# Kernel tuning notes

Hardware: AMD Instinct MI355X
Metric: run time of the kernel (lower is better)

Reference implementation:

```python
import jax, jax.numpy as jnp
import numpy as np


def _maxpool2(t):
    # 2x2 max pool, stride 2. t: [B, C, H, W]
    B, C, H, W = t.shape
    return t.reshape(B, C, H // 2, 2, W // 2, 2).max(axis=(3, 5))


def setup_inputs() -> dict:
    key = jax.random.key(0)
    ks = jax.random.split(key, 5)
    B, C, H, W = 4, 64, 128, 128
    x = jax.random.normal(ks[0], (B, C, H, W), dtype=jnp.float32)
    w_theta = jax.random.normal(ks[1], (C // 8, C), dtype=jnp.float32) * (1.0 / np.sqrt(C))
    w_phi = jax.random.normal(ks[2], (C // 8, C), dtype=jnp.float32) * (1.0 / np.sqrt(C))
    w_g = jax.random.normal(ks[3], (C // 2, C), dtype=jnp.float32) * (1.0 / np.sqrt(C))
    w_o = jax.random.normal(ks[4], (C, C // 2), dtype=jnp.float32) * (1.0 / np.sqrt(C // 2))
    gamma = jnp.ones((1,), dtype=jnp.float32)
    return {"x": x, "w_theta": w_theta, "w_phi": w_phi, "w_g": w_g, "w_o": w_o, "gamma": gamma}


def reference(x, w_theta, w_phi, w_g, w_o, gamma):
    B, C, H, W = x.shape
    N = H * W
    # 1x1 convs (bias-free) are channel matmuls
    theta = jnp.einsum('oc,bchw->bohw', w_theta, x)            # [B, C/8, H, W]
    phi = _maxpool2(jnp.einsum('oc,bchw->bohw', w_phi, x))     # [B, C/8, H/2, W/2]
    g = _maxpool2(jnp.einsum('oc,bchw->bohw', w_g, x))         # [B, C/2, H/2, W/2]
    theta = theta.reshape(B, C // 8, N)                        # [B, C/8, N]
    phi = phi.reshape(B, C // 8, N // 4)                       # [B, C/8, N/4]
    g = g.reshape(B, C // 2, N // 4)                           # [B, C/2, N/4]
    # attention: no 1/sqrt(d) scaling in SAGAN
    scores = jnp.einsum('bcn,bcm->bnm', theta, phi)            # [B, N, N/4]
    beta = jax.nn.softmax(scores, axis=-1)
    attn = jnp.einsum('bcm,bnm->bcn', g, beta)                 # [B, C/2, N]
    o = jnp.einsum('oc,bcn->bon', w_o, attn).reshape(B, C, H, W)
    return gamma[0] * o + x
```

## Files before the change

### kernel.cpp

```cpp
#include <hip/hip_runtime.h>
#include <hip/hip_bf16.h>


typedef __attribute__((ext_vector_type(16))) float f32x16;
typedef __attribute__((ext_vector_type(4))) float f32x4;
typedef __attribute__((ext_vector_type(2))) float f32x2;
typedef __attribute__((ext_vector_type(8))) short s16x8;

__device__ __forceinline__ unsigned short f32_bf16(float f) {
    unsigned int u = __float_as_uint(f);
    return (unsigned short)((u + 0x7fffu + ((u >> 16) & 1u)) >> 16);
}
__device__ __forceinline__ unsigned int pk_bf16(float a, float b) {
    return (unsigned int)f32_bf16(a) | ((unsigned int)f32_bf16(b) << 16);
}
__device__ __forceinline__ unsigned int pk_rh(float a, float b) {
    unsigned int au = __float_as_uint(a) + 0x8000u;
    unsigned int bu = __float_as_uint(b) + 0x8000u;
    return __builtin_amdgcn_perm(bu, au, 0x07060302u);
}
__device__ __forceinline__ unsigned int pk_tr(float a, float b) {
    return __builtin_amdgcn_perm(__float_as_uint(b), __float_as_uint(a), 0x07060302u);
}
__device__ __forceinline__ void async16(const void* g, void* l) {
    __builtin_amdgcn_global_load_lds(
        (const __attribute__((address_space(1))) unsigned int*)g,
        (__attribute__((address_space(3))) unsigned int*)l, 16, 0, 0);
}

__global__ __launch_bounds__(256) void proj_kernel(
    const float* __restrict__ x,
    const float* __restrict__ w_theta, const float* __restrict__ w_phi,
    const float* __restrict__ w_g,
    __hip_bfloat16* __restrict__ thG,
    __hip_bfloat16* __restrict__ phG,
    __hip_bfloat16* __restrict__ gG)
{
    __shared__ __align__(16) unsigned short x_s[128 * 72];
    int tid = threadIdx.x;
    int bx = blockIdx.x;
    int b = bx >> 7, mh = (bx >> 1) & 63, ph = bx & 1;

    {
        int cp = tid >> 3, s = tid & 7;
        const float* xb = x + ((size_t)b << 20) + (size_t)(2 * mh) * 128 + 64 * ph;
        const float* p0r = xb + ((size_t)(2 * cp) << 14);
        const float* p1r = p0r + (1 << 14);
#pragma unroll
        for (int py = 0; py < 2; py++)
#pragma unroll
            for (int t = 0; t < 2; t++) {
                int pxl = 4 * s + 32 * t;
                float4 a = *(const float4*)(p0r + py * 128 + pxl);
                float4 c = *(const float4*)(p1r + py * 128 + pxl);
                int pix = py * 64 + pxl;
                *(unsigned int*)&x_s[(pix + 0) * 72 + 2 * cp] = pk_rh(a.x, c.x);
                *(unsigned int*)&x_s[(pix + 1) * 72 + 2 * cp] = pk_rh(a.y, c.y);
                *(unsigned int*)&x_s[(pix + 2) * 72 + 2 * cp] = pk_rh(a.z, c.z);
                *(unsigned int*)&x_s[(pix + 3) * 72 + 2 * cp] = pk_rh(a.w, c.w);
            }
    }

    int lane = tid & 63, w = tid >> 6;
    int q = lane >> 4, nl = lane & 15;

    s16x8 A[3][2];
#pragma unroll
    for (int CT = 0; CT < 3; CT++) {
        const float* wsrc;
        float scale = 1.0f;
        if (CT == 0) {
            if (nl < 8) { wsrc = w_theta + nl * 64; scale = 1.44269504f; }
            else        { wsrc = w_phi + (nl - 8) * 64; }
        } else if (CT == 1) wsrc = w_g + nl * 64;
        else                wsrc = w_g + (16 + nl) * 64;
#pragma unroll
        for (int ks = 0; ks < 2; ks++) {
            const float4* p4 = (const float4*)(wsrc + 32 * ks + 8 * q);
            float4 a0 = p4[0], a1 = p4[1];
            s16x8 f;
            f[0] = (short)f32_bf16(a0.x * scale); f[1] = (short)f32_bf16(a0.y * scale);
            f[2] = (short)f32_bf16(a0.z * scale); f[3] = (short)f32_bf16(a0.w * scale);
            f[4] = (short)f32_bf16(a1.x * scale); f[5] = (short)f32_bf16(a1.y * scale);
            f[6] = (short)f32_bf16(a1.z * scale); f[7] = (short)f32_bf16(a1.w * scale);
            A[CT][ks] = f;
        }
    }
    __syncthreads();

    f32x4 acc[3][2];
#pragma unroll
    for (int ti = 0; ti < 2; ti++) {
        int tile = w + 4 * ti;
        const unsigned short* rb = x_s + (16 * tile + nl) * 72;
        s16x8 B0 = *(const s16x8*)(rb + 8 * q);
        s16x8 B1 = *(const s16x8*)(rb + 32 + 8 * q);
#pragma unroll
        for (int CT = 0; CT < 3; CT++) {
            f32x4 d = (f32x4){0.f, 0.f, 0.f, 0.f};
            d = __builtin_amdgcn_mfma_f32_16x16x32_bf16(A[CT][0], B0, d, 0, 0, 0);
            d = __builtin_amdgcn_mfma_f32_16x16x32_bf16(A[CT][1], B1, d, 0, 0, 0);
            acc[CT][ti] = d;
        }
    }

    if (q < 2) {
        unsigned short* thb = (unsigned short*)thG + ((size_t)b << 14) * 8;
#pragma unroll
        for (int ti = 0; ti < 2; ti++) {
            int n = (2 * mh + ti) * 128 + 64 * ph + 16 * w + nl;
            uint2 tv;
            tv.x = pk_bf16(acc[0][ti][0], acc[0][ti][1]);
            tv.y = pk_bf16(acc[0][ti][2], acc[0][ti][3]);
            *(uint2*)(thb + (size_t)n * 8 + 4 * q) = tv;
        }
    }

    float pool[3][4];
#pragma unroll
    for (int CT = 0; CT < 3; CT++)
#pragma unroll
        for (int r = 0; r < 4; r++) {
            float a = fmaxf(acc[CT][0][r], acc[CT][1][r]);
            pool[CT][r] = fmaxf(a, __shfl_xor(a, 1));
        }

    int mm = 8 * w + (nl >> 1);
    int mbase = mh * 64 + ph * 32;
    if ((nl & 1) == 0) {
        if (q >= 2) {
            uint2 pv;
            pv.x = pk_bf16(pool[0][0], pool[0][1]);
            pv.y = pk_bf16(pool[0][2], pool[0][3]);
            *(uint2*)((unsigned short*)phG + ((size_t)(b * 4096 + mbase + mm)) * 8 + (q - 2) * 4) = pv;
        }
        int p = 16 * ((mm >> 4) & 1) + 8 * ((mm >> 2) & 1) + 4 * ((mm >> 3) & 1) + (mm & 3);
        int mstore = mbase + p;
#pragma unroll
        for (int CT = 1; CT < 3; CT++)
#pragma unroll
            for (int r = 0; r < 4; r++) {
                int cg = 16 * (CT - 1) + 4 * q + r;
                ((unsigned short*)gG)[((size_t)(b * 32 + cg) << 12) + mstore] =
                    f32_bf16(pool[CT][r]);
            }
    }
}

__global__ __launch_bounds__(256) void attn_kernel(
    const __hip_bfloat16* __restrict__ thG, const __hip_bfloat16* __restrict__ phG,
    const __hip_bfloat16* __restrict__ gG,
    const float* __restrict__ w_o, const float* __restrict__ gamma,
    const float* __restrict__ x, float* __restrict__ out)
{
    __shared__ __align__(16) unsigned char smem[2 * 16384 + 2 * 4096];
    unsigned char* O_s = smem;

    int tid = threadIdx.x, lane = tid & 63, w = tid >> 6;
    int q = lane >> 4, nl = lane & 15;
    int c31 = lane & 31, h = lane >> 5;
    int bx = blockIdx.x;
    int b  = bx >> 7;
    int n0 = (bx & 127) << 7;
    int nw = n0 + w * 32;

    const unsigned short* thb = (const unsigned short*)thG + ((size_t)b << 14) * 8;
    const unsigned short* phb = (const unsigned short*)phG + ((size_t)b << 12) * 8;
    const unsigned short* ggb = (const unsigned short*)gG + ((size_t)b << 17);

    s16x8 BT = (s16x8){0, 0, 0, 0, 0, 0, 0, 0};
    if (h == 0) BT = *(const s16x8*)(thb + (size_t)(nw + c31) * 8);
    else        BT[0] = (short)0xC167;
    s16x8 Fc = (s16x8){0, 0, 0, 0, 0, 0, 0, 0};
    if (h == 1) Fc[0] = (short)0x3F80;

    f32x16 acc = {};
    f32x2  l2 = (f32x2){0.f, 0.f};

    int r0 = 8 * w + (lane >> 5);
    const unsigned short* gsrc0 = ggb + ((size_t)(r0 + 0) << 12) + 8 * ((lane & 31) ^ (r0 + 0));
    const unsigned short* gsrc1 = ggb + ((size_t)(r0 + 2) << 12) + 8 * ((lane & 31) ^ (r0 + 2));
    const unsigned short* gsrc2 = ggb + ((size_t)(r0 + 4) << 12) + 8 * ((lane & 31) ^ (r0 + 4));
    const unsigned short* gsrc3 = ggb + ((size_t)(r0 + 6) << 12) + 8 * ((lane & 31) ^ (r0 + 6));
    const unsigned short* psrc  = phb + (size_t)(w * 64 + lane) * 8;
    unsigned char* ldsg0 = smem + w * 4096;
    unsigned char* ldsg1 = ldsg0 + 1024;
    unsigned char* ldsg2 = ldsg0 + 2048;
    unsigned char* ldsg3 = ldsg0 + 3072;
    unsigned char* ldsp  = smem + 32768 + w * 1024;

    async16(gsrc0, ldsg0);
    async16(gsrc1, ldsg1);
    async16(gsrc2, ldsg2);
    async16(gsrc3, ldsg3);
    async16(psrc, ldsp);
    __syncthreads();

    for (int st = 0; st < 16; st++) {
        const unsigned char* gcur = smem + (st & 1) * 16384;
        const unsigned char* pcur = smem + 32768 + (st & 1) * 4096;
        if (st < 15) {
            int mo = (st + 1) << 8;
            int nb = (st + 1) & 1;
            async16(gsrc0 + mo, ldsg0 + nb * 16384);
            async16(gsrc1 + mo, ldsg1 + nb * 16384);
            async16(gsrc2 + mo, ldsg2 + nb * 16384);
            async16(gsrc3 + mo, ldsg3 + nb * 16384);
            async16(psrc + (size_t)mo * 8, ldsp + nb * 4096);
        }
#pragma unroll
        for (int t8 = 0; t8 < 8; t8++) {
            int mloc = t8 << 5;
            s16x8 F = Fc;
            if (h == 0) F = *(const s16x8*)(pcur + (mloc + c31) * 16);
            int s0 = (t8 << 2) + h;
            s16x8 G1 = *(const s16x8*)(gcur + c31 * 512 + (((s0 + 0) ^ c31) << 4));
            s16x8 G2 = *(const s16x8*)(gcur + c31 * 512 + (((s0 + 2) ^ c31) << 4));

            f32x16 z = {};
            f32x16 S = __builtin_amdgcn_mfma_f32_32x32x16_bf16(F, BT, z, 0, 0, 0);

            float p0  = __builtin_amdgcn_exp2f(S[0]);
            float p1  = __builtin_amdgcn_exp2f(S[1]);
            float p2  = __builtin_amdgcn_exp2f(S[2]);
            float p3  = __builtin_amdgcn_exp2f(S[3]);
            float p4  = __builtin_amdgcn_exp2f(S[4]);
            float p5  = __builtin_amdgcn_exp2f(S[5]);
            float p6  = __builtin_amdgcn_exp2f(S[6]);
            float p7  = __builtin_amdgcn_exp2f(S[7]);
            float p8  = __builtin_amdgcn_exp2f(S[8]);
            float p9  = __builtin_amdgcn_exp2f(S[9]);
            float p10 = __builtin_amdgcn_exp2f(S[10]);
            float p11 = __builtin_amdgcn_exp2f(S[11]);
            float p12 = __builtin_amdgcn_exp2f(S[12]);
            float p13 = __builtin_amdgcn_exp2f(S[13]);
            float p14 = __builtin_amdgcn_exp2f(S[14]);
            float p15 = __builtin_amdgcn_exp2f(S[15]);

            f32x2 u0 = (f32x2){p0, p1} + (f32x2){p2, p3};
            f32x2 u1 = (f32x2){p4, p5} + (f32x2){p6, p7};
            f32x2 u2 = (f32x2){p8, p9} + (f32x2){p10, p11};
            f32x2 u3 = (f32x2){p12, p13} + (f32x2){p14, p15};
            l2 += (u0 + u1) + (u2 + u3);

            uint4 ub1 = make_uint4(pk_tr(p0, p1), pk_tr(p2, p3),
                                   pk_tr(p4, p5), pk_tr(p6, p7));
            uint4 ub2 = make_uint4(pk_tr(p8, p9), pk_tr(p10, p11),
                                   pk_tr(p12, p13), pk_tr(p14, p15));
            s16x8 B1 = *(s16x8*)&ub1;
            s16x8 B2 = *(s16x8*)&ub2;

            acc = __builtin_amdgcn_mfma_f32_32x32x16_bf16(G1, B1, acc, 0, 0, 0);
            acc = __builtin_amdgcn_mfma_f32_32x32x16_bf16(G2, B2, acc, 0, 0, 0);
        }
        __syncthreads();
    }

    float l = l2[0] + l2[1];
    l += __shfl_xor(l, 32);
    float linv = 1.0f / l;
    acc *= linv;

    s16x8 WO[4];
#pragma unroll
    for (int g4 = 0; g4 < 4; g4++) {
        const float4* wr = (const float4*)(w_o + (size_t)(g4 * 16 + nl) * 32 + q * 8);
        float4 a0 = wr[0], a1 = wr[1];
        WO[g4][0] = (short)f32_bf16(a0.x); WO[g4][1] = (short)f32_bf16(a0.y);
        WO[g4][2] = (short)f32_bf16(a0.z); WO[g4][3] = (short)f32_bf16(a0.w);
        WO[g4][4] = (short)f32_bf16(a1.x); WO[g4][5] = (short)f32_bf16(a1.y);
        WO[g4][6] = (short)f32_bf16(a1.z); WO[g4][7] = (short)f32_bf16(a1.w);
    }
    float gam = gamma[0];

    int nloc = w * 32 + c31;
    {
#pragma unroll
        for (int g2 = 0; g2 < 4; g2++) {
            uint2 ov;
            ov.x = pk_bf16(acc[4 * g2 + 0], acc[4 * g2 + 1]);
            ov.y = pk_bf16(acc[4 * g2 + 2], acc[4 * g2 + 3]);
            *(uint2*)(O_s + nloc * 80 + 16 * g2 + 8 * h) = ov;
        }
    }
    int nloc0 = w * 32 + nl;
    int nloc1 = nloc0 + 16;
    s16x8 OB0 = *(const s16x8*)(O_s + nloc0 * 80 + q * 16);
    s16x8 OB1 = *(const s16x8*)(O_s + nloc1 * 80 + q * 16);
#pragma unroll
    for (int g4 = 0; g4 < 4; g4++) {
        f32x4 e0 = (f32x4){0.f, 0.f, 0.f, 0.f};
        f32x4 e1 = (f32x4){0.f, 0.f, 0.f, 0.f};
        e0 = __builtin_amdgcn_mfma_f32_16x16x32_bf16(WO[g4], OB0, e0, 0, 0, 0);
        e1 = __builtin_amdgcn_mfma_f32_16x16x32_bf16(WO[g4], OB1, e1, 0, 0, 0);
#pragma unroll
        for (int r = 0; r < 4; r++) {
            int cc = g4 * 16 + q * 4 + r;
            size_t gi0 = (((size_t)(b * 64 + cc)) << 14) + nw + nl;
            out[gi0] = gam * e0[r] + x[gi0];
            size_t gi1 = gi0 + 16;
            out[gi1] = gam * e1[r] + x[gi1];
        }
    }
}

extern "C" void kernel_launch(void* const* d_in, const int* in_sizes, int n_in,
                              void* d_out, int out_size, void* d_ws, size_t ws_size,
                              hipStream_t stream) {
    const float* x       = (const float*)d_in[0];
    const float* w_theta = (const float*)d_in[1];
    const float* w_phi   = (const float*)d_in[2];
    const float* w_g     = (const float*)d_in[3];
    const float* w_o     = (const float*)d_in[4];
    const float* gamma   = (const float*)d_in[5];
    float* out = (float*)d_out;

    __hip_bfloat16* thG = (__hip_bfloat16*)d_ws;
    __hip_bfloat16* phG = thG + 524288;
    __hip_bfloat16* gG  = phG + 131072;

    proj_kernel<<<512, 256, 0, stream>>>(x, w_theta, w_phi, w_g, thG, phG, gG);
    attn_kernel<<<512, 256, 0, stream>>>(thG, phG, gG, w_o, gamma, x, out);
}
```

Baseline: 127.5 us.

## Split attention key range across two wave groups per block and merge via LDS

The attention kernel now launches 512 threads per block, with two halves of four waves each processing half of the key/value range (split-K) for the same 128 query rows. Each half keeps its own double-buffered G/phi tiles in LDS, and at the end the second half writes its accumulators and row sums to LDS so the first half can combine them, normalize, and run the output projection. This doubles the number of waves per CU to hide MFMA and exp latency, at the cost of an extra LDS reduction, a barrier, and half the waves idling during the epilogue.

```diff
diff --git a/kernel.cpp b/kernel.cpp
--- a/kernel.cpp
+++ b/kernel.cpp
@@ -147,22 +147,22 @@
     }
 }
 
-__global__ __launch_bounds__(256) void attn_kernel(
+__global__ __launch_bounds__(512, 4) void attn_kernel(
     const __hip_bfloat16* __restrict__ thG, const __hip_bfloat16* __restrict__ phG,
     const __hip_bfloat16* __restrict__ gG,
     const float* __restrict__ w_o, const float* __restrict__ gamma,
     const float* __restrict__ x, float* __restrict__ out)
 {
-    __shared__ __align__(16) unsigned char smem[2 * 16384 + 2 * 4096];
-    unsigned char* O_s = smem;
+    __shared__ __align__(64) unsigned char smem[40960];
 
     int tid = threadIdx.x, lane = tid & 63, w = tid >> 6;
+    int w4 = w & 3, hf = w >> 2;
     int q = lane >> 4, nl = lane & 15;
     int c31 = lane & 31, h = lane >> 5;
     int bx = blockIdx.x;
     int b  = bx >> 7;
     int n0 = (bx & 127) << 7;
-    int nw = n0 + w * 32;
+    int nw = n0 + w4 * 32;
 
     const unsigned short* thb = (const unsigned short*)thG + ((size_t)b << 14) * 8;
     const unsigned short* phb = (const unsigned short*)phG + ((size_t)b << 12) * 8;
@@ -177,45 +177,40 @@
     f32x16 acc = {};
     f32x2  l2 = (f32x2){0.f, 0.f};
 
-    int r0 = 8 * w + (lane >> 5);
-    const unsigned short* gsrc0 = ggb + ((size_t)(r0 + 0) << 12) + 8 * ((lane & 31) ^ (r0 + 0));
-    const unsigned short* gsrc1 = ggb + ((size_t)(r0 + 2) << 12) + 8 * ((lane & 31) ^ (r0 + 2));
-    const unsigned short* gsrc2 = ggb + ((size_t)(r0 + 4) << 12) + 8 * ((lane & 31) ^ (r0 + 4));
-    const unsigned short* gsrc3 = ggb + ((size_t)(r0 + 6) << 12) + 8 * ((lane & 31) ^ (r0 + 6));
-    const unsigned short* psrc  = phb + (size_t)(w * 64 + lane) * 8;
-    unsigned char* ldsg0 = smem + w * 4096;
-    unsigned char* ldsg1 = ldsg0 + 1024;
-    unsigned char* ldsg2 = ldsg0 + 2048;
-    unsigned char* ldsg3 = ldsg0 + 3072;
-    unsigned char* ldsp  = smem + 32768 + w * 1024;
-
-    async16(gsrc0, ldsg0);
-    async16(gsrc1, ldsg1);
-    async16(gsrc2, ldsg2);
-    async16(gsrc3, ldsg3);
-    async16(psrc, ldsp);
+    int rA = 8 * w4 + (lane >> 4);
+    int rB = rA + 4;
+    const unsigned short* gsrcA = ggb + ((size_t)rA << 12) + (hf << 11)
+                                  + (((lane & 15) ^ (rA & 15)) << 3);
+    const unsigned short* gsrcB = ggb + ((size_t)rB << 12) + (hf << 11)
+                                  + (((lane & 15) ^ (rB & 15)) << 3);
+    const unsigned short* psrc  = phb + (size_t)((hf << 11) + w4 * 64 + lane) * 8;
+    unsigned char* gdst = smem + hf * 16384 + w4 * 2048;
+    unsigned char* pdst = smem + 32768 + hf * 4096 + w4 * 1024;
+
+    async16(gsrcA, gdst);
+    async16(gsrcB, gdst + 1024);
+    if (w4 < 2) async16(psrc, pdst);
     __syncthreads();
 
     for (int st = 0; st < 16; st++) {
-        const unsigned char* gcur = smem + (st & 1) * 16384;
-        const unsigned char* pcur = smem + 32768 + (st & 1) * 4096;
+        const unsigned char* gcur = smem + hf * 16384 + (st & 1) * 8192;
+        const unsigned char* pcur = smem + 32768 + hf * 4096 + (st & 1) * 2048;
         if (st < 15) {
-            int mo = (st + 1) << 8;
             int nb = (st + 1) & 1;
-            async16(gsrc0 + mo, ldsg0 + nb * 16384);
-            async16(gsrc1 + mo, ldsg1 + nb * 16384);
-            async16(gsrc2 + mo, ldsg2 + nb * 16384);
-            async16(gsrc3 + mo, ldsg3 + nb * 16384);
-            async16(psrc + (size_t)mo * 8, ldsp + nb * 4096);
-        }
-#pragma unroll
-        for (int t8 = 0; t8 < 8; t8++) {
+            int mo = (st + 1) << 7;
+            async16(gsrcA + mo, gdst + nb * 8192);
+            async16(gsrcB + mo, gdst + nb * 8192 + 1024);
+            if (w4 < 2) async16(psrc + (size_t)mo * 8, pdst + nb * 2048);
+        }
+#pragma unroll
+        for (int t8 = 0; t8 < 4; t8++) {
             int mloc = t8 << 5;
             s16x8 F = Fc;
             if (h == 0) F = *(const s16x8*)(pcur + (mloc + c31) * 16);
             int s0 = (t8 << 2) + h;
-            s16x8 G1 = *(const s16x8*)(gcur + c31 * 512 + (((s0 + 0) ^ c31) << 4));
-            s16x8 G2 = *(const s16x8*)(gcur + c31 * 512 + (((s0 + 2) ^ c31) << 4));
+            int m15 = c31 & 15;
+            s16x8 G1 = *(const s16x8*)(gcur + c31 * 256 + (((s0 + 0) ^ m15) << 4));
+            s16x8 G2 = *(const s16x8*)(gcur + c31 * 256 + (((s0 + 2) ^ m15) << 4));
 
             f32x16 z = {};
             f32x16 S = __builtin_amdgcn_mfma_f32_32x32x16_bf16(F, BT, z, 0, 0, 0);
@@ -258,23 +253,34 @@
 
     float l = l2[0] + l2[1];
     l += __shfl_xor(l, 32);
-    float linv = 1.0f / l;
-    acc *= linv;
-
-    s16x8 WO[4];
-#pragma unroll
-    for (int g4 = 0; g4 < 4; g4++) {
-        const float4* wr = (const float4*)(w_o + (size_t)(g4 * 16 + nl) * 32 + q * 8);
-        float4 a0 = wr[0], a1 = wr[1];
-        WO[g4][0] = (short)f32_bf16(a0.x); WO[g4][1] = (short)f32_bf16(a0.y);
-        WO[g4][2] = (short)f32_bf16(a0.z); WO[g4][3] = (short)f32_bf16(a0.w);
-        WO[g4][4] = (short)f32_bf16(a1.x); WO[g4][5] = (short)f32_bf16(a1.y);
-        WO[g4][6] = (short)f32_bf16(a1.z); WO[g4][7] = (short)f32_bf16(a1.w);
-    }
-    float gam = gamma[0];
-
-    int nloc = w * 32 + c31;
-    {
+
+    int idx = (w4 << 6) + lane;
+    if (hf == 1) {
+        *(f32x16*)(smem + idx * 64) = acc;
+        *(float*)(smem + 32768 + idx * 4) = l;
+    }
+    __syncthreads();
+    if (hf == 0) {
+        f32x16 accB = *(const f32x16*)(smem + idx * 64);
+        float lB = *(const float*)(smem + 32768 + idx * 4);
+        acc += accB;
+        float linv = 1.0f / (l + lB);
+        acc *= linv;
+
+        s16x8 WO[4];
+#pragma unroll
+        for (int g4 = 0; g4 < 4; g4++) {
+            const float4* wr = (const float4*)(w_o + (size_t)(g4 * 16 + nl) * 32 + q * 8);
+            float4 a0 = wr[0], a1 = wr[1];
+            WO[g4][0] = (short)f32_bf16(a0.x); WO[g4][1] = (short)f32_bf16(a0.y);
+            WO[g4][2] = (short)f32_bf16(a0.z); WO[g4][3] = (short)f32_bf16(a0.w);
+            WO[g4][4] = (short)f32_bf16(a1.x); WO[g4][5] = (short)f32_bf16(a1.y);
+            WO[g4][6] = (short)f32_bf16(a1.z); WO[g4][7] = (short)f32_bf16(a1.w);
+        }
+        float gam = gamma[0];
+
+        unsigned char* O_s = smem + 20480;
+        int nloc = w4 * 32 + c31;
 #pragma unroll
         for (int g2 = 0; g2 < 4; g2++) {
             uint2 ov;
@@ -282,24 +288,24 @@
             ov.y = pk_bf16(acc[4 * g2 + 2], acc[4 * g2 + 3]);
             *(uint2*)(O_s + nloc * 80 + 16 * g2 + 8 * h) = ov;
         }
-    }
-    int nloc0 = w * 32 + nl;
-    int nloc1 = nloc0 + 16;
-    s16x8 OB0 = *(const s16x8*)(O_s + nloc0 * 80 + q * 16);
-    s16x8 OB1 = *(const s16x8*)(O_s + nloc1 * 80 + q * 16);
-#pragma unroll
-    for (int g4 = 0; g4 < 4; g4++) {
-        f32x4 e0 = (f32x4){0.f, 0.f, 0.f, 0.f};
-        f32x4 e1 = (f32x4){0.f, 0.f, 0.f, 0.f};
-        e0 = __builtin_amdgcn_mfma_f32_16x16x32_bf16(WO[g4], OB0, e0, 0, 0, 0);
-        e1 = __builtin_amdgcn_mfma_f32_16x16x32_bf16(WO[g4], OB1, e1, 0, 0, 0);
-#pragma unroll
-        for (int r = 0; r < 4; r++) {
-            int cc = g4 * 16 + q * 4 + r;
-            size_t gi0 = (((size_t)(b * 64 + cc)) << 14) + nw + nl;
-            out[gi0] = gam * e0[r] + x[gi0];
-            size_t gi1 = gi0 + 16;
-            out[gi1] = gam * e1[r] + x[gi1];
+        int nloc0 = w4 * 32 + nl;
+        int nloc1 = nloc0 + 16;
+        s16x8 OB0 = *(const s16x8*)(O_s + nloc0 * 80 + q * 16);
+        s16x8 OB1 = *(const s16x8*)(O_s + nloc1 * 80 + q * 16);
+#pragma unroll
+        for (int g4 = 0; g4 < 4; g4++) {
+            f32x4 e0 = (f32x4){0.f, 0.f, 0.f, 0.f};
+            f32x4 e1 = (f32x4){0.f, 0.f, 0.f, 0.f};
+            e0 = __builtin_amdgcn_mfma_f32_16x16x32_bf16(WO[g4], OB0, e0, 0, 0, 0);
+            e1 = __builtin_amdgcn_mfma_f32_16x16x32_bf16(WO[g4], OB1, e1, 0, 0, 0);
+#pragma unroll
+            for (int r = 0; r < 4; r++) {
+                int cc = g4 * 16 + q * 4 + r;
+                size_t gi0 = (((size_t)(b * 64 + cc)) << 14) + nw + nl;
+                out[gi0] = gam * e0[r] + x[gi0];
+                size_t gi1 = gi0 + 16;
+                out[gi1] = gam * e1[r] + x[gi1];
+            }
         }
     }
 }
@@ -320,5 +326,5 @@
     __hip_bfloat16* gG  = phG + 131072;
 
     proj_kernel<<<512, 256, 0, stream>>>(x, w_theta, w_phi, w_g, thG, phG, gG);
-    attn_kernel<<<512, 256, 0, stream>>>(thG, phG, gG, w_o, gamma, x, out);
-}
+    attn_kernel<<<512, 512, 0, stream>>>(thG, phG, gG, w_o, gamma, x, out);
+}
```

After: 117.6 us (median of 2 runs). 7.8% less time.
